# Kernel optimization log

Measured on AMD Instinct MI355X. Metric: run time of the kernel, lower is better.

The kernel has to match this reference:

```python
import jax, jax.numpy as jnp
import numpy as np

B, L, D = 2, 2048, 1024
H, QK, V = 8, 128, 128
EPS = 1e-5  # torch GroupNorm default


def setup_inputs() -> dict:
    key = jax.random.key(0)
    ks = jax.random.split(key, 6)
    sequence = jax.random.normal(ks[0], (B, L, D), jnp.float32)
    times = jnp.broadcast_to(jnp.arange(L, dtype=jnp.float32), (B, L))
    shift = D ** -0.5
    scale = 2.0 * shift
    w_q = jax.random.uniform(ks[1], (H, D, QK), jnp.float32) * scale - shift
    w_k = jax.random.uniform(ks[2], (H, D, QK), jnp.float32) * scale - shift
    w_v = jax.random.uniform(ks[3], (H, D, V), jnp.float32) * scale - shift
    out_dims = H * V
    w_g = jax.random.uniform(ks[4], (D, out_dims), jnp.float32) * scale - shift
    shift2 = out_dims ** -0.5
    scale2 = 2.0 * shift2
    w_o = jax.random.uniform(ks[5], (out_dims, out_dims), jnp.float32) * scale2 - shift2
    gn_w = jnp.ones((out_dims,), jnp.float32)
    gn_b = jnp.zeros((out_dims,), jnp.float32)
    return dict(sequence=sequence, times=times, w_q=w_q, w_k=w_k, w_v=w_v,
                w_g=w_g, w_o=w_o, gn_w=gn_w, gn_b=gn_b)


def rotate_by_i(x):
    # pairs (even, odd) -> (-odd, even), interleaved back
    x2 = x.reshape(x.shape[:-1] + (-1, 2))
    real, imag = x2[..., 0], x2[..., 1]
    return jnp.stack([-imag, real], axis=-1).reshape(x.shape)


def reference(sequence, times, w_q, w_k, w_v, w_g, w_o, gn_w, gn_b):
    gammas = 1.0 - 2.0 ** (-5.0 - jnp.arange(H, dtype=jnp.float32))            # (H,)
    thetas = 10000.0 ** (-2.0 * jnp.arange(QK // 2, dtype=jnp.float32) / QK)   # (QK/2,)

    q = jnp.einsum('bld,hdk->hblk', sequence, w_q)  # (H,B,L,QK)
    k = jnp.einsum('bld,hdk->hblk', sequence, w_k)
    v = jnp.einsum('bld,hdv->hblv', sequence, w_v)  # (H,B,L,V)

    # xPos rotor: angles interleaved-duplicated along last dim
    angles = times[..., None] * thetas              # (B,L,QK/2)
    cos = jnp.repeat(jnp.cos(angles), 2, axis=-1)   # (B,L,QK)
    sin = jnp.repeat(jnp.sin(angles), 2, axis=-1)
    q = cos * q + sin * rotate_by_i(q)
    k = cos * k - sin * rotate_by_i(k)

    # causal exponential-decay mask D[n,m] = gamma**(n-m) * (n>=m)
    mat = times[:, :, None] - times[:, None, :]     # (B,L,L)
    mask = mat >= 0
    g4 = gammas[:, None, None, None]                # (H,1,1,1)
    d = jnp.where(mask, g4 ** jnp.where(mask, mat, 0.0), 0.0)  # (H,B,L,L)

    ret = jnp.einsum('hbik,hbjk->hbij', q, k) * d   # (H,B,L,L)
    retention = jnp.einsum('hbij,hbjv->hbiv', ret, v)  # (H,B,L,V)

    # GroupNorm(num_heads, H*V): normalize each head's V channels per token
    r = jnp.transpose(retention, (1, 2, 0, 3))      # (B,L,H,V)
    mean = r.mean(-1, keepdims=True)
    var = r.var(-1, keepdims=True)
    rn = (r - mean) / jnp.sqrt(var + EPS)
    rn = rn * gn_w.reshape(H, V) + gn_b.reshape(H, V)
    rn = rn.reshape(B, L, H * V)

    g = sequence @ w_g
    gate = g * jax.nn.sigmoid(g)                    # swish
    return (gate * rn) @ w_o                        # (B,L,H*V)
```

## Files before the change

kernel.cpp:

```cpp
#include <hip/hip_runtime.h>
#include <stdint.h>

typedef unsigned short u16;
typedef unsigned int   u32;
typedef short  short8 __attribute__((ext_vector_type(8)));
typedef float  f32x4  __attribute__((ext_vector_type(4)));

#define DEV static __device__ __forceinline__

DEV float bf2f(u16 u) { u32 x = ((u32)u) << 16; float f; __builtin_memcpy(&f, &x, 4); return f; }
DEV u16 f2bf(float f) {
  u32 u; __builtin_memcpy(&u, &f, 4);
  return (u16)((u + 0x7FFFu + ((u >> 16) & 1u)) >> 16);
}
DEV bool probe_bf16(const void* times) { return *(const u32*)times == 0x3F800000u; }

DEV void gload16(const u16* g, u16* l) {
  __builtin_amdgcn_global_load_lds(
      (__attribute__((address_space(1))) void*)(u16*)g,
      (__attribute__((address_space(3))) void*)l, 16, 0, 0);
}

DEV f32x4 MFMA(short8 a, short8 b, f32x4 c) {
  return __builtin_amdgcn_mfma_f32_16x16x32_bf16(a, b, c, 0, 0, 0);
}

DEV void gemm128(const u16* Ag, const u16* Bg, int K, u16* sA, u16* sB,
                 f32x4 (&acc)[4][4]) {
  const int tid = threadIdx.x;
  const int lane = tid & 63, w = tid >> 6;
  const int wm = w >> 1, wn = w & 1;
  const int row = lane & 15, quad = lane >> 4;
  f32x4 z = {0.f, 0.f, 0.f, 0.f};
#pragma unroll
  for (int mt = 0; mt < 4; ++mt)
#pragma unroll
    for (int nt = 0; nt < 4; ++nt) acc[mt][nt] = z;

  for (int k0 = 0; k0 < K; k0 += 64) {
    __syncthreads();
#pragma unroll
    for (int i = 0; i < 4; ++i) {
      int c = (w << 2) + i;
      gload16(Ag + (size_t)(c * 8 + (lane >> 3)) * K + k0 + (lane & 7) * 8, sA + c * 544);
      gload16(Bg + (size_t)(c * 8 + (lane >> 3)) * K + k0 + (lane & 7) * 8, sB + c * 544);
    }
    __syncthreads();
#pragma unroll
    for (int kt = 0; kt < 2; ++kt) {
      short8 av[4], bv[4];
#pragma unroll
      for (int t = 0; t < 4; ++t) {
        int m = wm * 64 + t * 16 + row;
        av[t] = *(const short8*)(sA + (m >> 3) * 544 + (m & 7) * 64 + kt * 32 + quad * 8);
        int n = wn * 64 + t * 16 + row;
        bv[t] = *(const short8*)(sB + (n >> 3) * 544 + (n & 7) * 64 + kt * 32 + quad * 8);
      }
#pragma unroll
      for (int mt = 0; mt < 4; ++mt)
#pragma unroll
        for (int nt = 0; nt < 4; ++nt)
          acc[mt][nt] = MFMA(av[mt], bv[nt], acc[mt][nt]);
    }
  }
}

__global__ __launch_bounds__(256) void transpose_kernel(
    const void* wq, const void* wk, const void* wv, const void* wg,
    const void* wo, const void* times, u16* wsT) {
  __shared__ u16 T[128 * 132];
  int s = blockIdx.x, t = blockIdx.y;
  bool isbf = probe_bf16(times);
  const void* src; int ld; size_t off0;
  if (s < 8)       { src = wq; ld = 128;  off0 = (size_t)s * 131072; }
  else if (s < 16) { src = wk; ld = 128;  off0 = (size_t)(s - 8) * 131072; }
  else if (s < 24) { src = wv; ld = 128;  off0 = (size_t)(s - 16) * 131072; }
  else if (s < 32) { src = wg; ld = 1024; off0 = (size_t)(s - 24) * 128; }
  else             { src = wo; ld = 1024; off0 = (size_t)(s - 32) * 128; }
  int d0 = t * 128;
  const u16* s16 = (const u16*)src;
  const float* s32 = (const float*)src;
  for (int pass = 0; pass < 64; ++pass) {
    int idx = pass * 256 + threadIdx.x;
    int dl = idx >> 7, c = idx & 127;
    size_t goff = off0 + (size_t)(d0 + dl) * ld + c;
    T[c * 132 + dl] = isbf ? s16[goff] : f2bf(s32[goff]);
  }
  __syncthreads();
  u16* dst = wsT + (size_t)s * 131072;
  for (int pass = 0; pass < 16; ++pass) {
    int idx = pass * 256 + threadIdx.x;
    int c = idx >> 5, ch = idx & 31;
    uint2 v = *(const uint2*)&T[c * 132 + ch * 4];
    *(uint2*)&dst[(size_t)c * 1024 + d0 + ch * 4] = v;
  }
}

__global__ __launch_bounds__(256) void seq_kernel(const void* seq, const void* times, u16* dst) {
  bool isbf = probe_bf16(times);
  size_t idx = ((size_t)blockIdx.x * 256 + threadIdx.x) * 8;
  if (isbf) {
    *(uint4*)&dst[idx] = *(const uint4*)((const u16*)seq + idx);
  } else {
    const float* s = (const float*)seq;
    u32 a0 = (u32)f2bf(s[idx + 0]) | ((u32)f2bf(s[idx + 1]) << 16);
    u32 a1 = (u32)f2bf(s[idx + 2]) | ((u32)f2bf(s[idx + 3]) << 16);
    u32 a2 = (u32)f2bf(s[idx + 4]) | ((u32)f2bf(s[idx + 5]) << 16);
    u32 a3 = (u32)f2bf(s[idx + 6]) | ((u32)f2bf(s[idx + 7]) << 16);
    uint4 v; v.x = a0; v.y = a1; v.z = a2; v.w = a3;
    *(uint4*)&dst[idx] = v;
  }
}

__global__ __launch_bounds__(256, 2) void proj_kernel(
    const u16* seqb, const void* times, const u16* wsT,
    u16* qws, u16* kws, u16* vtws, u16* gatews) {
  __shared__ __align__(16) u16 smem[17408];
  u16* sA = smem;
  u16* sB = smem + 8704;
  int nb = blockIdx.x, mb = blockIdx.y;
  f32x4 acc[4][4];
  gemm128(seqb + (size_t)mb * 128 * 1024, wsT + (size_t)nb * 131072, 1024, sA, sB, acc);

  const int tid = threadIdx.x, lane = tid & 63, w = tid >> 6;
  const int wm = w >> 1, wn = w & 1, row = lane & 15, quad = lane >> 4;
  const bool isbf = probe_bf16(times);
  const u16* t16 = (const u16*)times;
  const float* t32 = (const float*)times;
  const int b = mb >> 4, l0 = (mb & 15) * 128;

  __syncthreads();

  if (nb < 16) {
    int type = nb >> 3;
    int h = nb & 7;
    float sgnk = type ? -1.f : 1.f;
#pragma unroll
    for (int mt = 0; mt < 4; ++mt) {
#pragma unroll
      for (int nt = 0; nt < 4; ++nt) {
        int c = wn * 64 + nt * 16 + row;
        float theta = exp2f(-0.2076205059304601f * (float)(c >> 1));
        float sgn = (c & 1) ? 1.f : -1.f;
#pragma unroll
        for (int r = 0; r < 4; ++r) {
          int lloc = wm * 64 + mt * 16 + quad * 4 + r;
          float v = acc[mt][nt][r];
          float pv = __shfl_xor(v, 1);
          float tv = isbf ? bf2f(t16[b * 2048 + l0 + lloc]) : t32[b * 2048 + l0 + lloc];
          float rev = theta * tv * 0.15915494309189535f;
          rev -= floorf(rev);
          float sn = __builtin_amdgcn_sinf(rev);
          float cs = __builtin_amdgcn_cosf(rev);
          float ov = cs * v + sgnk * sgn * sn * pv;
          u16 o16 = f2bf(ov);
          int other = __shfl_xor((int)o16, 1);
          if (!(lane & 1))
            *(u32*)&smem[lloc * 136 + c] = (u32)o16 | ((u32)other << 16);
        }
      }
    }
    __syncthreads();
    u16* outp = (type ? kws : qws) + (((size_t)(h * 2 + b) * 2048 + l0) << 7);
#pragma unroll
    for (int p = 0; p < 8; ++p) {
      int idx = p * 256 + tid, rr = idx >> 4, ch = idx & 15;
      *(uint4*)&outp[(size_t)rr * 128 + ch * 8] = *(const uint4*)&smem[rr * 136 + ch * 8];
    }
  } else if (nb < 24) {
    int h = nb & 7;
#pragma unroll
    for (int mt = 0; mt < 4; ++mt) {
      int lb = wm * 64 + mt * 16 + quad * 4;
#pragma unroll
      for (int nt = 0; nt < 4; ++nt) {
        int c = wn * 64 + nt * 16 + row;
        uint2 pk;
        pk.x = (u32)f2bf(acc[mt][nt][0]) | ((u32)f2bf(acc[mt][nt][1]) << 16);
        pk.y = (u32)f2bf(acc[mt][nt][2]) | ((u32)f2bf(acc[mt][nt][3]) << 16);
        *(uint2*)&smem[c * 136 + lb] = pk;
      }
    }
    __syncthreads();
    u16* outp = vtws + (size_t)(h * 2 + b) * 262144 + l0;
#pragma unroll
    for (int p = 0; p < 8; ++p) {
      int idx = p * 256 + tid, cc = idx >> 4, ch = idx & 15;
      *(uint4*)&outp[(size_t)cc * 2048 + ch * 8] = *(const uint4*)&smem[cc * 136 + ch * 8];
    }
  } else {
    int cb = nb - 24;
#pragma unroll
    for (int mt = 0; mt < 4; ++mt) {
#pragma unroll
      for (int nt = 0; nt < 4; ++nt) {
        int c = wn * 64 + nt * 16 + row;
#pragma unroll
        for (int r = 0; r < 4; ++r) {
          int lloc = wm * 64 + mt * 16 + quad * 4 + r;
          float x = acc[mt][nt][r];
          float s = x / (1.f + __expf(-x));
          u16 o16 = f2bf(s);
          int other = __shfl_xor((int)o16, 1);
          if (!(lane & 1))
            *(u32*)&smem[lloc * 136 + c] = (u32)o16 | ((u32)other << 16);
        }
      }
    }
    __syncthreads();
    u16* outp = gatews + (size_t)(mb * 128) * 1024 + (size_t)cb * 128;
#pragma unroll
    for (int p = 0; p < 8; ++p) {
      int idx = p * 256 + tid, rr = idx >> 4, ch = idx & 15;
      *(uint4*)&outp[(size_t)rr * 1024 + ch * 8] = *(const uint4*)&smem[rr * 136 + ch * 8];
    }
  }
}

__global__ __launch_bounds__(256, 1) void retention_kernel(
    const u16* qws, const u16* kws, const u16* vtws, const void* times, float* rws) {
  __shared__ __align__(16) u16 sK[32 * 528];
  __shared__ __align__(16) u16 sV[32 * 528];
  __shared__ __align__(16) u16 sP[128 * 136];
  const int ib = blockIdx.x, hb = blockIdx.y;
  const int h = hb >> 1, b = hb & 1;
  const int i0 = ib * 128;
  const int tid = threadIdx.x, lane = tid & 63, w = tid >> 6;
  const int wm = w >> 1, wn = w & 1, row = lane & 15, quad = lane >> 4;
  const bool isbf = probe_bf16(times);
  const u16* t16 = (const u16*)times;
  const float* t32 = (const float*)times;
  const float gamma = 1.f - exp2f(-5.f - (float)h);
  const float l2g = log2f(gamma);

  short8 qf[4][4];
  const u16* qbase = qws + ((size_t)hb * 2048 + i0) * 128;
#pragma unroll
  for (int mt = 0; mt < 4; ++mt)
#pragma unroll
    for (int kt = 0; kt < 4; ++kt)
      qf[mt][kt] = *(const short8*)(qbase + (size_t)(wm * 64 + mt * 16 + row) * 128 + kt * 32 + quad * 8);

  float trow[4][4], rpow[4][4];
#pragma unroll
  for (int mt = 0; mt < 4; ++mt)
#pragma unroll
    for (int r = 0; r < 4; ++r) {
      int i = i0 + wm * 64 + mt * 16 + quad * 4 + r;
      float tv = isbf ? bf2f(t16[b * 2048 + i]) : t32[b * 2048 + i];
      trow[mt][r] = tv;
      rpow[mt][r] = exp2f(l2g * (tv - (float)i0));
    }

  f32x4 z = {0.f, 0.f, 0.f, 0.f};
  f32x4 oacc[4][4];
#pragma unroll
  for (int mt = 0; mt < 4; ++mt)
#pragma unroll
    for (int nt = 0; nt < 4; ++nt) oacc[mt][nt] = z;

  const u16* kbase = kws + (size_t)hb * 262144;
  const u16* vbase = vtws + (size_t)hb * 262144;

  for (int jb = 0; jb <= ib; ++jb) {
    const int j0 = jb * 128;
    if (l2g * (float)(i0 - j0 - 258) < -57.f) continue;
    __syncthreads();
#pragma unroll
    for (int ii = 0; ii < 8; ++ii) {
      int c = w * 8 + ii;
      gload16(kbase + (size_t)(j0 + c * 4 + (lane >> 4)) * 128 + (lane & 15) * 8, sK + c * 528);
      gload16(vbase + (size_t)(c * 4 + (lane >> 4)) * 2048 + j0 + (lane & 15) * 8, sV + c * 528);
    }
    __syncthreads();

    f32x4 p[4][4];
#pragma unroll
    for (int mt = 0; mt < 4; ++mt)
#pragma unroll
      for (int nt = 0; nt < 4; ++nt) p[mt][nt] = z;
#pragma unroll
    for (int kt = 0; kt < 4; ++kt) {
      short8 bv[4];
#pragma unroll
      for (int nt = 0; nt < 4; ++nt) {
        int jr = wn * 64 + nt * 16 + row;
        bv[nt] = *(const short8*)(sK + (jr >> 2) * 528 + (jr & 3) * 128 + kt * 32 + quad * 8);
      }
#pragma unroll
      for (int mt = 0; mt < 4; ++mt)
#pragma unroll
        for (int nt = 0; nt < 4; ++nt)
          p[mt][nt] = MFMA(qf[mt][kt], bv[nt], p[mt][nt]);
    }

    float tcol[4], cp[4];
#pragma unroll
    for (int nt = 0; nt < 4; ++nt) {
      int j = j0 + wn * 64 + nt * 16 + row;
      float tv = isbf ? bf2f(t16[b * 2048 + j]) : t32[b * 2048 + j];
      tcol[nt] = tv;
      cp[nt] = exp2f(l2g * ((float)i0 - tv));
    }
    bool intra = (jb == ib);
#pragma unroll
    for (int mt = 0; mt < 4; ++mt)
#pragma unroll
      for (int nt = 0; nt < 4; ++nt)
#pragma unroll
        for (int r = 0; r < 4; ++r) {
          float f = rpow[mt][r] * cp[nt];
          float val = p[mt][nt][r] * f;
          if (intra && (trow[mt][r] < tcol[nt])) val = 0.f;
          sP[(wm * 64 + mt * 16 + quad * 4 + r) * 136 + wn * 64 + nt * 16 + row] = f2bf(val);
        }
    __syncthreads();

#pragma unroll
    for (int kt = 0; kt < 4; ++kt) {
      short8 av[4], bv[4];
#pragma unroll
      for (int mt = 0; mt < 4; ++mt)
        av[mt] = *(const short8*)(sP + (wm * 64 + mt * 16 + row) * 136 + kt * 32 + quad * 8);
#pragma unroll
      for (int nt = 0; nt < 4; ++nt) {
        int v = wn * 64 + nt * 16 + row;
        bv[nt] = *(const short8*)(sV + (v >> 2) * 528 + (v & 3) * 128 + kt * 32 + quad * 8);
      }
#pragma unroll
      for (int mt = 0; mt < 4; ++mt)
#pragma unroll
        for (int nt = 0; nt < 4; ++nt)
          oacc[mt][nt] = MFMA(av[mt], bv[nt], oacc[mt][nt]);
    }
  }

#pragma unroll
  for (int mt = 0; mt < 4; ++mt)
#pragma unroll
    for (int nt = 0; nt < 4; ++nt)
#pragma unroll
      for (int r = 0; r < 4; ++r) {
        int i = i0 + wm * 64 + mt * 16 + quad * 4 + r;
        int v = wn * 64 + nt * 16 + row;
        rws[((size_t)hb * 2048 + i) * 128 + v] = oacc[mt][nt][r];
      }
}

__global__ __launch_bounds__(256) void norm_kernel(
    const float* rws, const u16* gatews, const void* gnw, const void* gnb,
    const void* times, u16* xws) {
  int tid = threadIdx.x, lane = tid & 63, w = tid >> 6;
  int rid = blockIdx.x * 4 + w;
  int hb = rid >> 11, l = rid & 2047, h = hb >> 1, b = hb & 1;
  bool isbf = probe_bf16(times);
  float2 xv = *(const float2*)&rws[(size_t)rid * 128 + lane * 2];
  float s = xv.x + xv.y, ss = xv.x * xv.x + xv.y * xv.y;
#pragma unroll
  for (int o = 1; o < 64; o <<= 1) { s += __shfl_xor(s, o); ss += __shfl_xor(ss, o); }
  float mean = s * (1.f / 128.f);
  float var = fmaxf(ss * (1.f / 128.f) - mean * mean, 0.f);
  float inv = rsqrtf(var + 1e-5f);
  int c0 = h * 128 + lane * 2;
  float g0, g1, bb0, bb1;
  if (isbf) {
    g0 = bf2f(((const u16*)gnw)[c0]); g1 = bf2f(((const u16*)gnw)[c0 + 1]);
    bb0 = bf2f(((const u16*)gnb)[c0]); bb1 = bf2f(((const u16*)gnb)[c0 + 1]);
  } else {
    g0 = ((const float*)gnw)[c0]; g1 = ((const float*)gnw)[c0 + 1];
    bb0 = ((const float*)gnb)[c0]; bb1 = ((const float*)gnb)[c0 + 1];
  }
  float y0 = (xv.x - mean) * inv * g0 + bb0;
  float y1 = (xv.y - mean) * inv * g1 + bb1;
  size_t xi = ((size_t)(b * 2048 + l)) * 1024 + c0;
  float gt0 = bf2f(gatews[xi]), gt1 = bf2f(gatews[xi + 1]);
  u32 pk = (u32)f2bf(y0 * gt0) | ((u32)f2bf(y1 * gt1) << 16);
  *(u32*)&xws[xi] = pk;
}

__global__ __launch_bounds__(256, 2) void out_kernel(
    const u16* xws, const u16* wsT, const void* times, void* dout) {
  __shared__ __align__(16) u16 smem[17408];
  u16* sA = smem;
  u16* sB = smem + 8704;
  int nb = blockIdx.x, mb = blockIdx.y;
  f32x4 acc[4][4];
  gemm128(xws + (size_t)mb * 128 * 1024, wsT + (size_t)(32 + nb) * 131072, 1024, sA, sB, acc);
  const int tid = threadIdx.x, lane = tid & 63, w = tid >> 6;
  const int wm = w >> 1, wn = w & 1, row = lane & 15, quad = lane >> 4;
  bool isbf = probe_bf16(times);
  if (isbf) {
    __syncthreads();
#pragma unroll
    for (int mt = 0; mt < 4; ++mt) {
#pragma unroll
      for (int nt = 0; nt < 4; ++nt) {
        int c = wn * 64 + nt * 16 + row;
#pragma unroll
        for (int r = 0; r < 4; ++r) {
          int lloc = wm * 64 + mt * 16 + quad * 4 + r;
          u16 o16 = f2bf(acc[mt][nt][r]);
          int other = __shfl_xor((int)o16, 1);
          if (!(lane & 1))
            *(u32*)&smem[lloc * 136 + c] = (u32)o16 | ((u32)other << 16);
        }
      }
    }
    __syncthreads();
    u16* outp = (u16*)dout + (size_t)(mb * 128) * 1024 + (size_t)nb * 128;
#pragma unroll
    for (int p = 0; p < 8; ++p) {
      int idx = p * 256 + tid, rr = idx >> 4, ch = idx & 15;
      *(uint4*)&outp[(size_t)rr * 1024 + ch * 8] = *(const uint4*)&smem[rr * 136 + ch * 8];
    }
  } else {
#pragma unroll
    for (int mt = 0; mt < 4; ++mt)
#pragma unroll
      for (int nt = 0; nt < 4; ++nt)
#pragma unroll
        for (int r = 0; r < 4; ++r) {
          int i = mb * 128 + wm * 64 + mt * 16 + quad * 4 + r;
          size_t o = (size_t)i * 1024 + nb * 128 + wn * 64 + nt * 16 + row;
          ((float*)dout)[o] = acc[mt][nt][r];
        }
  }
}

extern "C" void kernel_launch(void* const* d_in, const int* in_sizes, int n_in,
                              void* d_out, int out_size, void* d_ws, size_t ws_size,
                              hipStream_t stream) {
  const void* seq   = d_in[0];
  const void* times = d_in[1];
  const void* wq = d_in[2];
  const void* wk = d_in[3];
  const void* wv = d_in[4];
  const void* wg = d_in[5];
  const void* wo = d_in[6];
  const void* gnw = d_in[7];
  const void* gnb = d_in[8];

  u16* ws = (u16*)d_ws;
  u16* wsT    = ws;
  u16* qws    = ws + 5242880;
  u16* kws    = qws + 4194304;
  u16* vtws   = kws + 4194304;
  u16* gatews = vtws + 4194304;
  float* rws  = (float*)(gatews + 4194304);
  u16* seqb   = (u16*)(rws + 4194304);
  u16* xws    = qws;

  transpose_kernel<<<dim3(40, 8), 256, 0, stream>>>(wq, wk, wv, wg, wo, times, wsT);
  seq_kernel<<<dim3(2048), 256, 0, stream>>>(seq, times, seqb);
  proj_kernel<<<dim3(32, 32), 256, 0, stream>>>(seqb, times, wsT, qws, kws, vtws, gatews);
  retention_kernel<<<dim3(16, 16), 256, 0, stream>>>(qws, kws, vtws, times, rws);
  norm_kernel<<<dim3(8192), 256, 0, stream>>>(rws, gatews, gnw, gnb, times, xws);
  out_kernel<<<dim3(8, 32), 256, 0, stream>>>(xws, wsT, times, d_out);
}
```

Before: 273.0 us.

## Split long retention rows across two blocks and share K/P LDS buffer

Retention blocks for the later 8 query tiles now split their causal key-block range into two halves handled by separate blocks. The second half writes a partial result to a separate buffer that norm_kernel adds back in. The K tile and the P tile now share one LDS buffer, with an extra barrier between them, so LDS use drops and two blocks can run per CU. Launch bounds on the projection and output GEMMs are raised to 4. The aim is to fix load imbalance across the triangular workload and raise occupancy, at the cost of extra partial-sum traffic, an added barrier, and possible register pressure or spills.

```diff
diff --git a/kernel.cpp b/kernel.cpp
--- a/kernel.cpp
+++ b/kernel.cpp
@@ -112,7 +112,7 @@
   }
 }
 
-__global__ __launch_bounds__(256, 2) void proj_kernel(
+__global__ __launch_bounds__(256, 4) void proj_kernel(
     const u16* seqb, const void* times, const u16* wsT,
     u16* qws, u16* kws, u16* vtws, u16* gatews) {
   __shared__ __align__(16) u16 smem[17408];
@@ -217,12 +217,22 @@
   }
 }
 
-__global__ __launch_bounds__(256, 1) void retention_kernel(
-    const u16* qws, const u16* kws, const u16* vtws, const void* times, float* rws) {
-  __shared__ __align__(16) u16 sK[32 * 528];
+__global__ __launch_bounds__(256, 2) void retention_kernel(
+    const u16* qws, const u16* kws, const u16* vtws, const void* times,
+    float* rws, float* rws2) {
+  __shared__ __align__(16) u16 sKP[128 * 132];
   __shared__ __align__(16) u16 sV[32 * 528];
-  __shared__ __align__(16) u16 sP[128 * 136];
-  const int ib = blockIdx.x, hb = blockIdx.y;
+  const int bx = blockIdx.x, hb = blockIdx.y;
+  int ib, jb_lo, jb_hi;
+  bool second;
+  if (bx < 8) { ib = bx; jb_lo = 0; jb_hi = ib + 1; second = false; }
+  else {
+    int idx = bx - 8;
+    ib = 8 + (idx >> 1);
+    int nj = ib + 1, mid = nj >> 1;
+    if ((idx & 1) == 0) { jb_lo = 0;   jb_hi = mid; second = false; }
+    else                { jb_lo = mid; jb_hi = nj;  second = true;  }
+  }
   const int h = hb >> 1, b = hb & 1;
   const int i0 = ib * 128;
   const int tid = threadIdx.x, lane = tid & 63, w = tid >> 6;
@@ -262,14 +272,14 @@
   const u16* kbase = kws + (size_t)hb * 262144;
   const u16* vbase = vtws + (size_t)hb * 262144;
 
-  for (int jb = 0; jb <= ib; ++jb) {
+  for (int jb = jb_lo; jb < jb_hi; ++jb) {
     const int j0 = jb * 128;
     if (l2g * (float)(i0 - j0 - 258) < -57.f) continue;
     __syncthreads();
 #pragma unroll
     for (int ii = 0; ii < 8; ++ii) {
       int c = w * 8 + ii;
-      gload16(kbase + (size_t)(j0 + c * 4 + (lane >> 4)) * 128 + (lane & 15) * 8, sK + c * 528);
+      gload16(kbase + (size_t)(j0 + c * 4 + (lane >> 4)) * 128 + (lane & 15) * 8, sKP + c * 528);
       gload16(vbase + (size_t)(c * 4 + (lane >> 4)) * 2048 + j0 + (lane & 15) * 8, sV + c * 528);
     }
     __syncthreads();
@@ -285,7 +295,7 @@
 #pragma unroll
       for (int nt = 0; nt < 4; ++nt) {
         int jr = wn * 64 + nt * 16 + row;
-        bv[nt] = *(const short8*)(sK + (jr >> 2) * 528 + (jr & 3) * 128 + kt * 32 + quad * 8);
+        bv[nt] = *(const short8*)(sKP + (jr >> 2) * 528 + (jr & 3) * 128 + kt * 32 + quad * 8);
       }
 #pragma unroll
       for (int mt = 0; mt < 4; ++mt)
@@ -303,6 +313,7 @@
       cp[nt] = exp2f(l2g * ((float)i0 - tv));
     }
     bool intra = (jb == ib);
+    __syncthreads();
 #pragma unroll
     for (int mt = 0; mt < 4; ++mt)
 #pragma unroll
@@ -312,7 +323,7 @@
           float f = rpow[mt][r] * cp[nt];
           float val = p[mt][nt][r] * f;
           if (intra && (trow[mt][r] < tcol[nt])) val = 0.f;
-          sP[(wm * 64 + mt * 16 + quad * 4 + r) * 136 + wn * 64 + nt * 16 + row] = f2bf(val);
+          sKP[(wm * 64 + mt * 16 + quad * 4 + r) * 132 + wn * 64 + nt * 16 + row] = f2bf(val);
         }
     __syncthreads();
 
@@ -321,7 +332,7 @@
       short8 av[4], bv[4];
 #pragma unroll
       for (int mt = 0; mt < 4; ++mt)
-        av[mt] = *(const short8*)(sP + (wm * 64 + mt * 16 + row) * 136 + kt * 32 + quad * 8);
+        av[mt] = *(const short8*)(sKP + (wm * 64 + mt * 16 + row) * 132 + kt * 32 + quad * 8);
 #pragma unroll
       for (int nt = 0; nt < 4; ++nt) {
         int v = wn * 64 + nt * 16 + row;
@@ -343,18 +354,25 @@
       for (int r = 0; r < 4; ++r) {
         int i = i0 + wm * 64 + mt * 16 + quad * 4 + r;
         int v = wn * 64 + nt * 16 + row;
-        rws[((size_t)hb * 2048 + i) * 128 + v] = oacc[mt][nt][r];
+        if (second)
+          rws2[((size_t)hb * 1024 + (i - 1024)) * 128 + v] = oacc[mt][nt][r];
+        else
+          rws[((size_t)hb * 2048 + i) * 128 + v] = oacc[mt][nt][r];
       }
 }
 
 __global__ __launch_bounds__(256) void norm_kernel(
-    const float* rws, const u16* gatews, const void* gnw, const void* gnb,
-    const void* times, u16* xws) {
+    const float* rws, const float* rws2, const u16* gatews,
+    const void* gnw, const void* gnb, const void* times, u16* xws) {
   int tid = threadIdx.x, lane = tid & 63, w = tid >> 6;
   int rid = blockIdx.x * 4 + w;
   int hb = rid >> 11, l = rid & 2047, h = hb >> 1, b = hb & 1;
   bool isbf = probe_bf16(times);
   float2 xv = *(const float2*)&rws[(size_t)rid * 128 + lane * 2];
+  if (l >= 1024) {
+    float2 x2 = *(const float2*)&rws2[((size_t)hb * 1024 + (l - 1024)) * 128 + lane * 2];
+    xv.x += x2.x; xv.y += x2.y;
+  }
   float s = xv.x + xv.y, ss = xv.x * xv.x + xv.y * xv.y;
 #pragma unroll
   for (int o = 1; o < 64; o <<= 1) { s += __shfl_xor(s, o); ss += __shfl_xor(ss, o); }
@@ -378,7 +396,7 @@
   *(u32*)&xws[xi] = pk;
 }
 
-__global__ __launch_bounds__(256, 2) void out_kernel(
+__global__ __launch_bounds__(256, 4) void out_kernel(
     const u16* xws, const u16* wsT, const void* times, void* dout) {
   __shared__ __align__(16) u16 smem[17408];
   u16* sA = smem;
@@ -448,12 +466,13 @@
   u16* gatews = vtws + 4194304;
   float* rws  = (float*)(gatews + 4194304);
   u16* seqb   = (u16*)(rws + 4194304);
+  float* rws2 = (float*)seqb;
   u16* xws    = qws;
 
   transpose_kernel<<<dim3(40, 8), 256, 0, stream>>>(wq, wk, wv, wg, wo, times, wsT);
   seq_kernel<<<dim3(2048), 256, 0, stream>>>(seq, times, seqb);
   proj_kernel<<<dim3(32, 32), 256, 0, stream>>>(seqb, times, wsT, qws, kws, vtws, gatews);
-  retention_kernel<<<dim3(16, 16), 256, 0, stream>>>(qws, kws, vtws, times, rws);
-  norm_kernel<<<dim3(8192), 256, 0, stream>>>(rws, gatews, gnw, gnb, times, xws);
+  retention_kernel<<<dim3(24, 16), 256, 0, stream>>>(qws, kws, vtws, times, rws, rws2);
+  norm_kernel<<<dim3(8192), 256, 0, stream>>>(rws, rws2, gatews, gnw, gnb, times, xws);
   out_kernel<<<dim3(8, 32), 256, 0, stream>>>(xws, wsT, times, d_out);
 }
```

After: 287.4 us. +5.3%, slower.

## Split retention into per-wave 32-row tiles with split-K partials reduced in norm

Applied to the files above, without the earlier changes.

The retention kernel now gives each wavefront a 32-row query tile. Long causal rows are split into 2 or 3 chunks along the key dimension for load balance, and the partial outputs go to reused workspace buffers that the norm kernel sums. K and V fragments are read straight from global memory instead of being staged in shared memory with block barriers, and the decay cutoff skip now works at 32-column granularity. The projection and output GEMMs also get a higher occupancy hint in launch_bounds. The intent is to remove triangular load imbalance and barrier stalls, at the cost of less LDS reuse of K/V, more global traffic and extra partial-sum reads in norm.

```diff
diff --git a/kernel.cpp b/kernel.cpp
--- a/kernel.cpp
+++ b/kernel.cpp
@@ -112,7 +112,7 @@
   }
 }
 
-__global__ __launch_bounds__(256, 2) void proj_kernel(
+__global__ __launch_bounds__(256, 4) void proj_kernel(
     const u16* seqb, const void* times, const u16* wsT,
     u16* qws, u16* kws, u16* vtws, u16* gatews) {
   __shared__ __align__(16) u16 smem[17408];
@@ -217,144 +217,164 @@
   }
 }
 
-__global__ __launch_bounds__(256, 1) void retention_kernel(
-    const u16* qws, const u16* kws, const u16* vtws, const void* times, float* rws) {
-  __shared__ __align__(16) u16 sK[32 * 528];
-  __shared__ __align__(16) u16 sV[32 * 528];
-  __shared__ __align__(16) u16 sP[128 * 136];
-  const int ib = blockIdx.x, hb = blockIdx.y;
+__global__ __launch_bounds__(256) void retention_kernel(
+    const u16* qws, const u16* kws, const u16* vtws, const void* times,
+    float* rws, float* part0, float* part1) {
+  __shared__ __align__(16) u16 sP[4][1280];
+  const int tid = threadIdx.x, lane = tid & 63, w = tid >> 6;
+  const int row = lane & 15, quad = lane >> 4;
+  u16* myP = &sP[w][0];
+
+  const int wid = blockIdx.x * 4 + w;
+  const int hb = wid / 126;
+  const int cid = 125 - (wid % 126);
+  int itile, idx, nc;
+  if (cid < 22)      { itile = cid; idx = 0; nc = 1; }
+  else if (cid < 66) { itile = 22 + ((cid - 22) >> 1); idx = (cid - 22) & 1; nc = 2; }
+  else { int x = cid - 66; int q3 = (x * 171) >> 9; itile = 44 + q3; idx = x - 3 * q3; nc = 3; }
+  const int n = itile + 1;
+  int lo, hi;
+  if (nc == 1)      { lo = 0;                      hi = n; }
+  else if (nc == 2) { lo = (idx * n) >> 1;         hi = ((idx + 1) * n) >> 1; }
+  else              { lo = (idx * n * 171) >> 9;   hi = ((idx + 1) * n * 171) >> 9; }
+
   const int h = hb >> 1, b = hb & 1;
-  const int i0 = ib * 128;
-  const int tid = threadIdx.x, lane = tid & 63, w = tid >> 6;
-  const int wm = w >> 1, wn = w & 1, row = lane & 15, quad = lane >> 4;
+  const int i0 = itile * 32;
   const bool isbf = probe_bf16(times);
-  const u16* t16 = (const u16*)times;
-  const float* t32 = (const float*)times;
+  const u16* t16 = (const u16*)times + b * 2048;
+  const float* t32 = (const float*)times + b * 2048;
   const float gamma = 1.f - exp2f(-5.f - (float)h);
   const float l2g = log2f(gamma);
 
-  short8 qf[4][4];
+  short8 qf[2][4];
   const u16* qbase = qws + ((size_t)hb * 2048 + i0) * 128;
 #pragma unroll
-  for (int mt = 0; mt < 4; ++mt)
+  for (int ii = 0; ii < 2; ++ii)
 #pragma unroll
     for (int kt = 0; kt < 4; ++kt)
-      qf[mt][kt] = *(const short8*)(qbase + (size_t)(wm * 64 + mt * 16 + row) * 128 + kt * 32 + quad * 8);
-
-  float trow[4][4], rpow[4][4];
-#pragma unroll
-  for (int mt = 0; mt < 4; ++mt)
-#pragma unroll
-    for (int r = 0; r < 4; ++r) {
-      int i = i0 + wm * 64 + mt * 16 + quad * 4 + r;
-      float tv = isbf ? bf2f(t16[b * 2048 + i]) : t32[b * 2048 + i];
-      trow[mt][r] = tv;
-      rpow[mt][r] = exp2f(l2g * (tv - (float)i0));
-    }
+      qf[ii][kt] = *(const short8*)(qbase + (size_t)(ii * 16 + row) * 128 + kt * 32 + quad * 8);
+
+  float tiv[2];
+#pragma unroll
+  for (int ii = 0; ii < 2; ++ii)
+    tiv[ii] = isbf ? bf2f(t16[i0 + ii * 16 + row]) : t32[i0 + ii * 16 + row];
 
   f32x4 z = {0.f, 0.f, 0.f, 0.f};
-  f32x4 oacc[4][4];
-#pragma unroll
-  for (int mt = 0; mt < 4; ++mt)
-#pragma unroll
-    for (int nt = 0; nt < 4; ++nt) oacc[mt][nt] = z;
+  f32x4 oacc[2][8];
+#pragma unroll
+  for (int mt = 0; mt < 2; ++mt)
+#pragma unroll
+    for (int vt = 0; vt < 8; ++vt) oacc[mt][vt] = z;
 
   const u16* kbase = kws + (size_t)hb * 262144;
   const u16* vbase = vtws + (size_t)hb * 262144;
 
-  for (int jb = 0; jb <= ib; ++jb) {
-    const int j0 = jb * 128;
-    if (l2g * (float)(i0 - j0 - 258) < -57.f) continue;
-    __syncthreads();
-#pragma unroll
-    for (int ii = 0; ii < 8; ++ii) {
-      int c = w * 8 + ii;
-      gload16(kbase + (size_t)(j0 + c * 4 + (lane >> 4)) * 128 + (lane & 15) * 8, sK + c * 528);
-      gload16(vbase + (size_t)(c * 4 + (lane >> 4)) * 2048 + j0 + (lane & 15) * 8, sV + c * 528);
-    }
-    __syncthreads();
-
-    f32x4 p[4][4];
-#pragma unroll
-    for (int mt = 0; mt < 4; ++mt)
-#pragma unroll
-      for (int nt = 0; nt < 4; ++nt) p[mt][nt] = z;
+  for (int jt = lo; jt < hi; ++jt) {
+    const int j0 = jt * 32;
+    if (l2g * (float)(i0 - j0 - 47) < -57.f) continue;
+
+    f32x4 pt[2][2];
+#pragma unroll
+    for (int jj = 0; jj < 2; ++jj)
+#pragma unroll
+      for (int ii = 0; ii < 2; ++ii) pt[jj][ii] = z;
 #pragma unroll
     for (int kt = 0; kt < 4; ++kt) {
-      short8 bv[4];
-#pragma unroll
-      for (int nt = 0; nt < 4; ++nt) {
-        int jr = wn * 64 + nt * 16 + row;
-        bv[nt] = *(const short8*)(sK + (jr >> 2) * 528 + (jr & 3) * 128 + kt * 32 + quad * 8);
-      }
-#pragma unroll
-      for (int mt = 0; mt < 4; ++mt)
-#pragma unroll
-        for (int nt = 0; nt < 4; ++nt)
-          p[mt][nt] = MFMA(qf[mt][kt], bv[nt], p[mt][nt]);
-    }
-
-    float tcol[4], cp[4];
-#pragma unroll
-    for (int nt = 0; nt < 4; ++nt) {
-      int j = j0 + wn * 64 + nt * 16 + row;
-      float tv = isbf ? bf2f(t16[b * 2048 + j]) : t32[b * 2048 + j];
-      tcol[nt] = tv;
-      cp[nt] = exp2f(l2g * ((float)i0 - tv));
-    }
-    bool intra = (jb == ib);
-#pragma unroll
-    for (int mt = 0; mt < 4; ++mt)
-#pragma unroll
-      for (int nt = 0; nt < 4; ++nt)
-#pragma unroll
-        for (int r = 0; r < 4; ++r) {
-          float f = rpow[mt][r] * cp[nt];
-          float val = p[mt][nt][r] * f;
-          if (intra && (trow[mt][r] < tcol[nt])) val = 0.f;
-          sP[(wm * 64 + mt * 16 + quad * 4 + r) * 136 + wn * 64 + nt * 16 + row] = f2bf(val);
+      short8 kf0 = *(const short8*)(kbase + (size_t)(j0 + row) * 128 + kt * 32 + quad * 8);
+      short8 kf1 = *(const short8*)(kbase + (size_t)(j0 + 16 + row) * 128 + kt * 32 + quad * 8);
+      pt[0][0] = MFMA(kf0, qf[0][kt], pt[0][0]);
+      pt[0][1] = MFMA(kf0, qf[1][kt], pt[0][1]);
+      pt[1][0] = MFMA(kf1, qf[0][kt], pt[1][0]);
+      pt[1][1] = MFMA(kf1, qf[1][kt], pt[1][1]);
+    }
+
+    const float j0f = (float)j0;
+    const float rpo0 = exp2f(l2g * (tiv[0] - j0f));
+    const float rpo1 = exp2f(l2g * (tiv[1] - j0f));
+    const bool diag = (jt == itile);
+#pragma unroll
+    for (int jj = 0; jj < 2; ++jj) {
+      float tj[4];
+      if (isbf) {
+        uint2 tp = *(const uint2*)&t16[j0 + jj * 16 + quad * 4];
+        tj[0] = bf2f((u16)tp.x); tj[1] = bf2f((u16)(tp.x >> 16));
+        tj[2] = bf2f((u16)tp.y); tj[3] = bf2f((u16)(tp.y >> 16));
+      } else {
+        f32x4 tp = *(const f32x4*)&t32[j0 + jj * 16 + quad * 4];
+        tj[0] = tp[0]; tj[1] = tp[1]; tj[2] = tp[2]; tj[3] = tp[3];
+      }
+      float cp[4];
+#pragma unroll
+      for (int r = 0; r < 4; ++r) cp[r] = exp2f(l2g * (j0f - tj[r]));
+#pragma unroll
+      for (int ii = 0; ii < 2; ++ii) {
+        float rp = ii ? rpo1 : rpo0;
+        float ti = tiv[ii];
+        float v0 = pt[jj][ii][0] * rp * cp[0];
+        float v1 = pt[jj][ii][1] * rp * cp[1];
+        float v2 = pt[jj][ii][2] * rp * cp[2];
+        float v3 = pt[jj][ii][3] * rp * cp[3];
+        if (diag) {
+          if (ti < tj[0]) v0 = 0.f;
+          if (ti < tj[1]) v1 = 0.f;
+          if (ti < tj[2]) v2 = 0.f;
+          if (ti < tj[3]) v3 = 0.f;
         }
-    __syncthreads();
-
-#pragma unroll
-    for (int kt = 0; kt < 4; ++kt) {
-      short8 av[4], bv[4];
-#pragma unroll
-      for (int mt = 0; mt < 4; ++mt)
-        av[mt] = *(const short8*)(sP + (wm * 64 + mt * 16 + row) * 136 + kt * 32 + quad * 8);
-#pragma unroll
-      for (int nt = 0; nt < 4; ++nt) {
-        int v = wn * 64 + nt * 16 + row;
-        bv[nt] = *(const short8*)(sV + (v >> 2) * 528 + (v & 3) * 128 + kt * 32 + quad * 8);
-      }
-#pragma unroll
-      for (int mt = 0; mt < 4; ++mt)
-#pragma unroll
-        for (int nt = 0; nt < 4; ++nt)
-          oacc[mt][nt] = MFMA(av[mt], bv[nt], oacc[mt][nt]);
-    }
-  }
-
-#pragma unroll
-  for (int mt = 0; mt < 4; ++mt)
-#pragma unroll
-    for (int nt = 0; nt < 4; ++nt)
-#pragma unroll
-      for (int r = 0; r < 4; ++r) {
-        int i = i0 + wm * 64 + mt * 16 + quad * 4 + r;
-        int v = wn * 64 + nt * 16 + row;
-        rws[((size_t)hb * 2048 + i) * 128 + v] = oacc[mt][nt][r];
-      }
+        uint2 pk;
+        pk.x = (u32)f2bf(v0) | ((u32)f2bf(v1) << 16);
+        pk.y = (u32)f2bf(v2) | ((u32)f2bf(v3) << 16);
+        *(uint2*)&myP[(ii * 16 + row) * 40 + jj * 16 + quad * 4] = pk;
+      }
+    }
+
+    short8 a0 = *(const short8*)&myP[(row) * 40 + quad * 8];
+    short8 a1 = *(const short8*)&myP[(16 + row) * 40 + quad * 8];
+#pragma unroll
+    for (int vt = 0; vt < 8; ++vt) {
+      short8 vb = *(const short8*)(vbase + (size_t)(vt * 16 + row) * 2048 + j0 + quad * 8);
+      oacc[0][vt] = MFMA(a0, vb, oacc[0][vt]);
+      oacc[1][vt] = MFMA(a1, vb, oacc[1][vt]);
+    }
+  }
+
+  float* dst;
+  if (idx == 0) {
+    dst = rws + ((size_t)hb * 2048 + i0) * 128;
+  } else {
+    int s_in = (itile < 44) ? (itile - 22) : (22 + (itile - 44) * 2 + (idx - 1));
+    int s = hb * 62 + s_in;
+    dst = (s < 512) ? part0 + (size_t)s * 4096 : part1 + (size_t)(s - 512) * 4096;
+  }
+#pragma unroll
+  for (int mt = 0; mt < 2; ++mt)
+#pragma unroll
+    for (int vt = 0; vt < 8; ++vt)
+#pragma unroll
+      for (int r = 0; r < 4; ++r)
+        dst[(size_t)(mt * 16 + quad * 4 + r) * 128 + vt * 16 + row] = oacc[mt][vt][r];
 }
 
 __global__ __launch_bounds__(256) void norm_kernel(
-    const float* rws, const u16* gatews, const void* gnw, const void* gnb,
-    const void* times, u16* xws) {
+    const float* rws, const float* part0, const float* part1, const u16* gatews,
+    const void* gnw, const void* gnb, const void* times, u16* xws) {
   int tid = threadIdx.x, lane = tid & 63, w = tid >> 6;
   int rid = blockIdx.x * 4 + w;
   int hb = rid >> 11, l = rid & 2047, h = hb >> 1, b = hb & 1;
   bool isbf = probe_bf16(times);
   float2 xv = *(const float2*)&rws[(size_t)rid * 128 + lane * 2];
+  int it = l >> 5;
+  if (it >= 22) {
+    int s = hb * 62 + ((it < 44) ? (it - 22) : (22 + (it - 44) * 2));
+    const float* pp = (s < 512) ? part0 + (size_t)s * 4096 : part1 + (size_t)(s - 512) * 4096;
+    float2 x2 = *(const float2*)&pp[(l & 31) * 128 + lane * 2];
+    xv.x += x2.x; xv.y += x2.y;
+    if (it >= 44) {
+      int s2 = s + 1;
+      const float* pp2 = (s2 < 512) ? part0 + (size_t)s2 * 4096 : part1 + (size_t)(s2 - 512) * 4096;
+      float2 x3 = *(const float2*)&pp2[(l & 31) * 128 + lane * 2];
+      xv.x += x3.x; xv.y += x3.y;
+    }
+  }
   float s = xv.x + xv.y, ss = xv.x * xv.x + xv.y * xv.y;
 #pragma unroll
   for (int o = 1; o < 64; o <<= 1) { s += __shfl_xor(s, o); ss += __shfl_xor(ss, o); }
@@ -378,7 +398,7 @@
   *(u32*)&xws[xi] = pk;
 }
 
-__global__ __launch_bounds__(256, 2) void out_kernel(
+__global__ __launch_bounds__(256, 4) void out_kernel(
     const u16* xws, const u16* wsT, const void* times, void* dout) {
   __shared__ __align__(16) u16 smem[17408];
   u16* sA = smem;
@@ -448,12 +468,14 @@
   u16* gatews = vtws + 4194304;
   float* rws  = (float*)(gatews + 4194304);
   u16* seqb   = (u16*)(rws + 4194304);
+  float* part0 = (float*)seqb;
+  float* part1 = (float*)wsT;
   u16* xws    = qws;
 
   transpose_kernel<<<dim3(40, 8), 256, 0, stream>>>(wq, wk, wv, wg, wo, times, wsT);
   seq_kernel<<<dim3(2048), 256, 0, stream>>>(seq, times, seqb);
   proj_kernel<<<dim3(32, 32), 256, 0, stream>>>(seqb, times, wsT, qws, kws, vtws, gatews);
-  retention_kernel<<<dim3(16, 16), 256, 0, stream>>>(qws, kws, vtws, times, rws);
-  norm_kernel<<<dim3(8192), 256, 0, stream>>>(rws, gatews, gnw, gnb, times, xws);
+  retention_kernel<<<dim3(504), 256, 0, stream>>>(qws, kws, vtws, times, rws, part0, part1);
+  norm_kernel<<<dim3(8192), 256, 0, stream>>>(rws, part0, part1, gatews, gnw, gnb, times, xws);
   out_kernel<<<dim3(8, 32), 256, 0, stream>>>(xws, wsT, times, d_out);
 }
```

Measured after the change: 284.8 us. +4.3%, slower.
